# Optimization experiments

Hardware: AMD Instinct MI355X
Metric: run time of the kernel (lower is better)

## Reference

```python
import jax, jax.numpy as jnp
import numpy as np

B, S, IN, HID = 8, 2048, 1024, 1024

def setup_inputs() -> dict:
    key = jax.random.key(0)
    ks = jax.random.split(key, 6)
    scale = 1.0 / np.sqrt(IN + HID)
    return {
        "x": jax.random.normal(ks[0], (B, S, IN), dtype=jnp.float32),
        "h": jax.random.normal(ks[1], (B, S, HID), dtype=jnp.float32),
        "W1": jax.random.normal(ks[2], (HID, IN + HID), dtype=jnp.float32) * scale,
        "b1": jax.random.normal(ks[3], (HID,), dtype=jnp.float32) * scale,
        "W2": jax.random.normal(ks[4], (HID, IN + HID), dtype=jnp.float32) * scale,
        "b2": jax.random.normal(ks[5], (HID,), dtype=jnp.float32) * scale,
    }

def reference(x, h, W1, b1, W2, b2):
    # combined1 = cat(x, h) ; forget = sigmoid(Linear1(combined1))
    combined1 = jnp.concatenate((x, h), axis=2)          # [B,S,IN+HID]
    forget = jax.nn.sigmoid(jnp.einsum('bsf,hf->bsh', combined1, W1) + b1)
    interim_h = forget * h                                # [B,S,HID]
    combined2 = jnp.concatenate((x, interim_h), axis=2)   # [B,S,IN+HID]
    interim_o = jnp.tanh(jnp.einsum('bsf,hf->bsh', combined2, W2) + b2)
    output = (1.0 - forget) * h + forget * interim_o
    return (output, output)
```

## Files before the change

### kernel.cpp

```cpp
#include <hip/hip_runtime.h>
#include <stdint.h>


#define M_ROWS 16384
#define K_DIM  2048
#define N_DIM  1024

typedef float  f32x4  __attribute__((ext_vector_type(4)));
typedef __bf16 bf16x8 __attribute__((ext_vector_type(8)));
typedef unsigned short u16x8 __attribute__((ext_vector_type(8)));

typedef __attribute__((address_space(3))) void as3_void;
typedef __attribute__((address_space(1))) void as1_void;

__device__ __forceinline__ void gload_lds16(const unsigned short* g, void* lds) {
    __builtin_amdgcn_global_load_lds((const as1_void*)g, (as3_void*)lds, 16, 0, 0);
}

__device__ __forceinline__ unsigned short f2bf(float f) {
    union { float f; unsigned u; } v; v.f = f;
    unsigned r = 0x7FFFu + ((v.u >> 16) & 1u);
    return (unsigned short)((v.u + r) >> 16);
}


__global__ void pack_A(const float* __restrict__ x, const float* __restrict__ h,
                       unsigned short* __restrict__ Abf) {
    size_t t = (size_t)blockIdx.x * blockDim.x + threadIdx.x;
    size_t e = t * 8;
    int row = (int)(e >> 11);
    int col = (int)(e & 2047);
    const float* src = (col < 1024) ? (x + (size_t)row * 1024 + col)
                                    : (h + (size_t)row * 1024 + (col - 1024));
    f32x4 v0 = ((const f32x4*)src)[0];
    f32x4 v1 = ((const f32x4*)src)[1];
    u16x8 o;
    o[0] = f2bf(v0[0]); o[1] = f2bf(v0[1]); o[2] = f2bf(v0[2]); o[3] = f2bf(v0[3]);
    o[4] = f2bf(v1[0]); o[5] = f2bf(v1[1]); o[6] = f2bf(v1[2]); o[7] = f2bf(v1[3]);
    *(u16x8*)(Abf + e) = o;
}

__global__ void pack_W(const float* __restrict__ W1, const float* __restrict__ W2,
                       unsigned short* __restrict__ W1b, unsigned short* __restrict__ W2b) {
    size_t t = (size_t)blockIdx.x * blockDim.x + threadIdx.x;
    size_t e = t * 8;
    int which = (int)(e >> 21);
    size_t e2 = e & ((1u << 21) - 1);
    const float* src = (which ? W2 : W1) + e2;
    unsigned short* dst = (which ? W2b : W1b) + e2;
    f32x4 v0 = ((const f32x4*)src)[0];
    f32x4 v1 = ((const f32x4*)src)[1];
    u16x8 o;
    o[0] = f2bf(v0[0]); o[1] = f2bf(v0[1]); o[2] = f2bf(v0[2]); o[3] = f2bf(v0[3]);
    o[4] = f2bf(v1[0]); o[5] = f2bf(v1[1]); o[6] = f2bf(v1[2]); o[7] = f2bf(v1[3]);
    *(u16x8*)dst = o;
}


__global__ __launch_bounds__(256) void gemm1(
        const unsigned short* __restrict__ Abf,
        const unsigned short* __restrict__ Wb,
        const float* __restrict__ bias,
        const float* __restrict__ h,
        float* Fout,
        unsigned short* __restrict__ H2)
{
    __shared__ unsigned short As[128 * 32];
    __shared__ unsigned short Bs[128 * 32];

    int bid = blockIdx.x;
    int wg  = (bid & 7) * 128 + (bid >> 3);
    int tn = wg & 7, tm = wg >> 3;
    int m0 = tm * 128, n0 = tn * 128;

    int t = threadIdx.x, wave = t >> 6, lane = t & 63;
    int wr = wave >> 1, wc = wave & 1;
    int fr = lane & 15, fq = lane >> 4;
    int sRow = t >> 2, sCol = (t & 3) * 8;

    const unsigned short* aBase = Abf + (size_t)(m0 + sRow) * K_DIM + sCol;
    const unsigned short* bBase = Wb  + (size_t)(n0 + sRow) * K_DIM + sCol;
    char* AsB = (char*)As;  char* BsB = (char*)Bs;
    int ldsW = wave * 1024;

    f32x4 acc[4][4] = {};

    for (int k0 = 0; k0 < K_DIM; k0 += 32) {
        gload_lds16(aBase + k0,                AsB + ldsW);
        gload_lds16(aBase + 64 * K_DIM + k0,   AsB + 4096 + ldsW);
        gload_lds16(bBase + k0,                BsB + ldsW);
        gload_lds16(bBase + 64 * K_DIM + k0,   BsB + 4096 + ldsW);
        __syncthreads();
        bf16x8 af[4], bfr[4];
#pragma unroll
        for (int i = 0; i < 4; i++) {
            af[i]  = *(const bf16x8*)&As[(wr * 64 + i * 16 + fr) * 32 + fq * 8];
            bfr[i] = *(const bf16x8*)&Bs[(wc * 64 + i * 16 + fr) * 32 + fq * 8];
        }
#pragma unroll
        for (int mi = 0; mi < 4; mi++)
#pragma unroll
            for (int ni = 0; ni < 4; ni++)
                acc[mi][ni] = __builtin_amdgcn_mfma_f32_16x16x32_bf16(
                                  af[mi], bfr[ni], acc[mi][ni], 0, 0, 0);
        __syncthreads();
    }

    int rowBase = m0 + wr * 64 + fq * 4;
    int colBase = n0 + wc * 64 + fr;
#pragma unroll
    for (int mi = 0; mi < 4; mi++) {
#pragma unroll
        for (int ni = 0; ni < 4; ni++) {
            int col = colBase + ni * 16;
            float b = bias[col];
#pragma unroll
            for (int j = 0; j < 4; j++) {
                int row = rowBase + mi * 16 + j;
                size_t idx = (size_t)row * N_DIM + col;
                float c = acc[mi][ni][j] + b;
                float f = 1.0f / (1.0f + expf(-c));
                Fout[idx] = f;
                float hv = h[idx];
                H2[idx] = f2bf(f * hv);
            }
        }
    }
}

__global__ __launch_bounds__(256) void gemm2(
        const unsigned short* __restrict__ Abf,
        const unsigned short* __restrict__ H2,
        const unsigned short* __restrict__ Wb,
        const float* __restrict__ bias,
        const float* __restrict__ h,
        float* Fout,
        float* Out2)
{
    __shared__ unsigned short As[128 * 32];
    __shared__ unsigned short Bs[128 * 32];

    int bid = blockIdx.x;
    int wg  = (bid & 7) * 128 + (bid >> 3);
    int tn = wg & 7, tm = wg >> 3;
    int m0 = tm * 128, n0 = tn * 128;

    int t = threadIdx.x, wave = t >> 6, lane = t & 63;
    int wr = wave >> 1, wc = wave & 1;
    int fr = lane & 15, fq = lane >> 4;
    int sRow = t >> 2, sCol = (t & 3) * 8;

    const unsigned short* aBase1 = Abf + (size_t)(m0 + sRow) * K_DIM + sCol;
    const unsigned short* aBase2 = H2  + (size_t)(m0 + sRow) * N_DIM + sCol;
    const unsigned short* bBase  = Wb  + (size_t)(n0 + sRow) * K_DIM + sCol;
    char* AsB = (char*)As;  char* BsB = (char*)Bs;
    int ldsW = wave * 1024;

    f32x4 acc[4][4] = {};

    for (int k0 = 0; k0 < K_DIM; k0 += 32) {
        if (k0 < 1024) {
            gload_lds16(aBase1 + k0,               AsB + ldsW);
            gload_lds16(aBase1 + 64 * K_DIM + k0,  AsB + 4096 + ldsW);
        } else {
            int kk = k0 - 1024;
            gload_lds16(aBase2 + kk,               AsB + ldsW);
            gload_lds16(aBase2 + 64 * N_DIM + kk,  AsB + 4096 + ldsW);
        }
        gload_lds16(bBase + k0,                BsB + ldsW);
        gload_lds16(bBase + 64 * K_DIM + k0,   BsB + 4096 + ldsW);
        __syncthreads();
        bf16x8 af[4], bfr[4];
#pragma unroll
        for (int i = 0; i < 4; i++) {
            af[i]  = *(const bf16x8*)&As[(wr * 64 + i * 16 + fr) * 32 + fq * 8];
            bfr[i] = *(const bf16x8*)&Bs[(wc * 64 + i * 16 + fr) * 32 + fq * 8];
        }
#pragma unroll
        for (int mi = 0; mi < 4; mi++)
#pragma unroll
            for (int ni = 0; ni < 4; ni++)
                acc[mi][ni] = __builtin_amdgcn_mfma_f32_16x16x32_bf16(
                                  af[mi], bfr[ni], acc[mi][ni], 0, 0, 0);
        __syncthreads();
    }

    int rowBase = m0 + wr * 64 + fq * 4;
    int colBase = n0 + wc * 64 + fr;
#pragma unroll
    for (int mi = 0; mi < 4; mi++) {
#pragma unroll
        for (int ni = 0; ni < 4; ni++) {
            int col = colBase + ni * 16;
            float b = bias[col];
#pragma unroll
            for (int j = 0; j < 4; j++) {
                int row = rowBase + mi * 16 + j;
                size_t idx = (size_t)row * N_DIM + col;
                float c = acc[mi][ni][j] + b;
                float o = tanhf(c);
                float f = Fout[idx];
                float hv = h[idx];
                float out = fmaf(f, o - hv, hv);
                Fout[idx] = out;
                Out2[idx] = out;
            }
        }
    }
}


extern "C" void kernel_launch(void* const* d_in, const int* in_sizes, int n_in,
                              void* d_out, int out_size, void* d_ws, size_t ws_size,
                              hipStream_t stream) {
    const float* x  = (const float*)d_in[0];
    const float* h  = (const float*)d_in[1];
    const float* W1 = (const float*)d_in[2];
    const float* b1 = (const float*)d_in[3];
    const float* W2 = (const float*)d_in[4];
    const float* b2 = (const float*)d_in[5];
    float* out = (float*)d_out;
    float* out2 = out + (size_t)M_ROWS * N_DIM;

    unsigned short* Abf = (unsigned short*)d_ws;
    unsigned short* H2  = (unsigned short*)((char*)d_ws + 67108864);
    unsigned short* W1b = (unsigned short*)((char*)d_ws + 100663296);
    unsigned short* W2b = (unsigned short*)((char*)d_ws + 104857600);

    pack_A<<<16384, 256, 0, stream>>>(x, h, Abf);
    pack_W<<<2048, 256, 0, stream>>>(W1, W2, W1b, W2b);
    gemm1<<<1024, 256, 0, stream>>>(Abf, W1b, b1, h, out, H2);
    gemm2<<<1024, 256, 0, stream>>>(Abf, H2, W2b, b2, h, out, out2);
}
```

Baseline: 537.5 us.

## Double-buffer LDS tiles in both GEMMs and raise MFMA wave priority

Both GEMM kernels now keep two LDS buffers for the A and B tiles. The next K-tile's global_load_lds is issued before the MFMA block on the current tile, so memory latency can overlap with matrix math. s_setprio is raised around the MFMA block. The XCD-aware block swizzle is also removed in favour of a plain row-major tile mapping, which changes how tiles are spread across L2 caches. LDS use per block doubles, which may lower occupancy.

Result: slower. 577.3 us (+7.4%).

```diff
diff --git a/kernel.cpp b/kernel.cpp
--- a/kernel.cpp
+++ b/kernel.cpp
@@ -57,6 +57,8 @@
 }
 
 
+#define NT (K_DIM / 32)
+
 __global__ __launch_bounds__(256) void gemm1(
         const unsigned short* __restrict__ Abf,
         const unsigned short* __restrict__ Wb,
@@ -65,46 +67,58 @@
         float* Fout,
         unsigned short* __restrict__ H2)
 {
-    __shared__ unsigned short As[128 * 32];
-    __shared__ unsigned short Bs[128 * 32];
+    __shared__ unsigned short As[2][4096];
+    __shared__ unsigned short Bs[2][4096];
 
     int bid = blockIdx.x;
-    int wg  = (bid & 7) * 128 + (bid >> 3);
-    int tn = wg & 7, tm = wg >> 3;
+    int tn = bid & 7, tm = bid >> 3;
     int m0 = tm * 128, n0 = tn * 128;
 
-    int t = threadIdx.x, wave = t >> 6, lane = t & 63;
+    int t = threadIdx.x, wave = t >> 6;
+    int lane = t & 63;
     int wr = wave >> 1, wc = wave & 1;
     int fr = lane & 15, fq = lane >> 4;
     int sRow = t >> 2, sCol = (t & 3) * 8;
 
     const unsigned short* aBase = Abf + (size_t)(m0 + sRow) * K_DIM + sCol;
     const unsigned short* bBase = Wb  + (size_t)(n0 + sRow) * K_DIM + sCol;
-    char* AsB = (char*)As;  char* BsB = (char*)Bs;
     int ldsW = wave * 1024;
 
+#define STAGE1(bufi, k0s)                                              \
+    do {                                                               \
+        char* AsB = (char*)As[bufi];  char* BsB = (char*)Bs[bufi];     \
+        gload_lds16(aBase + (k0s),                AsB + ldsW);         \
+        gload_lds16(aBase + 64 * K_DIM + (k0s),   AsB + 4096 + ldsW);  \
+        gload_lds16(bBase + (k0s),                BsB + ldsW);         \
+        gload_lds16(bBase + 64 * K_DIM + (k0s),   BsB + 4096 + ldsW);  \
+    } while (0)
+
     f32x4 acc[4][4] = {};
 
-    for (int k0 = 0; k0 < K_DIM; k0 += 32) {
-        gload_lds16(aBase + k0,                AsB + ldsW);
-        gload_lds16(aBase + 64 * K_DIM + k0,   AsB + 4096 + ldsW);
-        gload_lds16(bBase + k0,                BsB + ldsW);
-        gload_lds16(bBase + 64 * K_DIM + k0,   BsB + 4096 + ldsW);
-        __syncthreads();
+    STAGE1(0, 0);
+    __syncthreads();
+
+    int cur = 0;
+    for (int ti = 0; ti < NT; ++ti) {
+        if (ti + 1 < NT) STAGE1(cur ^ 1, (ti + 1) * 32);
         bf16x8 af[4], bfr[4];
 #pragma unroll
         for (int i = 0; i < 4; i++) {
-            af[i]  = *(const bf16x8*)&As[(wr * 64 + i * 16 + fr) * 32 + fq * 8];
-            bfr[i] = *(const bf16x8*)&Bs[(wc * 64 + i * 16 + fr) * 32 + fq * 8];
-        }
+            af[i]  = *(const bf16x8*)&As[cur][(wr * 64 + i * 16 + fr) * 32 + fq * 8];
+            bfr[i] = *(const bf16x8*)&Bs[cur][(wc * 64 + i * 16 + fr) * 32 + fq * 8];
+        }
+        __builtin_amdgcn_s_setprio(1);
 #pragma unroll
         for (int mi = 0; mi < 4; mi++)
 #pragma unroll
             for (int ni = 0; ni < 4; ni++)
                 acc[mi][ni] = __builtin_amdgcn_mfma_f32_16x16x32_bf16(
                                   af[mi], bfr[ni], acc[mi][ni], 0, 0, 0);
+        __builtin_amdgcn_s_setprio(0);
         __syncthreads();
-    }
+        cur ^= 1;
+    }
+#undef STAGE1
 
     int rowBase = m0 + wr * 64 + fq * 4;
     int colBase = n0 + wc * 64 + fr;
@@ -137,15 +151,15 @@
         float* Fout,
         float* Out2)
 {
-    __shared__ unsigned short As[128 * 32];
-    __shared__ unsigned short Bs[128 * 32];
+    __shared__ unsigned short As[2][4096];
+    __shared__ unsigned short Bs[2][4096];
 
     int bid = blockIdx.x;
-    int wg  = (bid & 7) * 128 + (bid >> 3);
-    int tn = wg & 7, tm = wg >> 3;
+    int tn = bid & 7, tm = bid >> 3;
     int m0 = tm * 128, n0 = tn * 128;
 
-    int t = threadIdx.x, wave = t >> 6, lane = t & 63;
+    int t = threadIdx.x, wave = t >> 6;
+    int lane = t & 63;
     int wr = wave >> 1, wc = wave & 1;
     int fr = lane & 15, fq = lane >> 4;
     int sRow = t >> 2, sCol = (t & 3) * 8;
@@ -153,37 +167,49 @@
     const unsigned short* aBase1 = Abf + (size_t)(m0 + sRow) * K_DIM + sCol;
     const unsigned short* aBase2 = H2  + (size_t)(m0 + sRow) * N_DIM + sCol;
     const unsigned short* bBase  = Wb  + (size_t)(n0 + sRow) * K_DIM + sCol;
-    char* AsB = (char*)As;  char* BsB = (char*)Bs;
     int ldsW = wave * 1024;
 
+#define STAGE2(bufi, k0s)                                                   \
+    do {                                                                    \
+        char* AsB = (char*)As[bufi];  char* BsB = (char*)Bs[bufi];          \
+        if ((k0s) < 1024) {                                                 \
+            gload_lds16(aBase1 + (k0s),               AsB + ldsW);          \
+            gload_lds16(aBase1 + 64 * K_DIM + (k0s),  AsB + 4096 + ldsW);   \
+        } else {                                                            \
+            int kk = (k0s) - 1024;                                          \
+            gload_lds16(aBase2 + kk,                  AsB + ldsW);          \
+            gload_lds16(aBase2 + 64 * N_DIM + kk,     AsB + 4096 + ldsW);   \
+        }                                                                   \
+        gload_lds16(bBase + (k0s),                BsB + ldsW);              \
+        gload_lds16(bBase + 64 * K_DIM + (k0s),   BsB + 4096 + ldsW);       \
+    } while (0)
+
     f32x4 acc[4][4] = {};
 
-    for (int k0 = 0; k0 < K_DIM; k0 += 32) {
-        if (k0 < 1024) {
-            gload_lds16(aBase1 + k0,               AsB + ldsW);
-            gload_lds16(aBase1 + 64 * K_DIM + k0,  AsB + 4096 + ldsW);
-        } else {
-            int kk = k0 - 1024;
-            gload_lds16(aBase2 + kk,               AsB + ldsW);
-            gload_lds16(aBase2 + 64 * N_DIM + kk,  AsB + 4096 + ldsW);
-        }
-        gload_lds16(bBase + k0,                BsB + ldsW);
-        gload_lds16(bBase + 64 * K_DIM + k0,   BsB + 4096 + ldsW);
-        __syncthreads();
+    STAGE2(0, 0);
+    __syncthreads();
+
+    int cur = 0;
+    for (int ti = 0; ti < NT; ++ti) {
+        if (ti + 1 < NT) STAGE2(cur ^ 1, (ti + 1) * 32);
         bf16x8 af[4], bfr[4];
 #pragma unroll
         for (int i = 0; i < 4; i++) {
-            af[i]  = *(const bf16x8*)&As[(wr * 64 + i * 16 + fr) * 32 + fq * 8];
-            bfr[i] = *(const bf16x8*)&Bs[(wc * 64 + i * 16 + fr) * 32 + fq * 8];
-        }
+            af[i]  = *(const bf16x8*)&As[cur][(wr * 64 + i * 16 + fr) * 32 + fq * 8];
+            bfr[i] = *(const bf16x8*)&Bs[cur][(wc * 64 + i * 16 + fr) * 32 + fq * 8];
+        }
+        __builtin_amdgcn_s_setprio(1);
 #pragma unroll
         for (int mi = 0; mi < 4; mi++)
 #pragma unroll
             for (int ni = 0; ni < 4; ni++)
                 acc[mi][ni] = __builtin_amdgcn_mfma_f32_16x16x32_bf16(
                                   af[mi], bfr[ni], acc[mi][ni], 0, 0, 0);
+        __builtin_amdgcn_s_setprio(0);
         __syncthreads();
-    }
+        cur ^= 1;
+    }
+#undef STAGE2
 
     int rowBase = m0 + wr * 64 + fq * 4;
     int colBase = n0 + wc * 64 + fr;
```
